# Optimization experiments

Hardware: AMD Instinct MI355X
Metric: run time of the kernel (lower is better)

Reference implementation:

```python
import jax, jax.numpy as jnp
import numpy as np
from jax import lax

N_NODES = 100000
N_EDGES = 1600000
FEAT = 8          # per-node feature dim
STATE = 4         # embed_dim
OUT = 16          # n classes
HID = 5           # hardcoded state_l1/output_l1
MAX_IT = 10


def setup_inputs() -> dict:
    key = jax.random.key(0)
    ks = jax.random.split(key, 12)
    edge_parent = jax.random.randint(ks[0], (N_EDGES,), 0, N_NODES, dtype=jnp.int32)
    edge_child = jax.random.randint(ks[1], (N_EDGES,), 0, N_NODES, dtype=jnp.int32)
    # arc_feat = inp[:, 1:] = [child_id, feat_parent, feat_child]  -> [E, 1+2F]
    feats = jax.random.normal(ks[2], (N_EDGES, 2 * FEAT), jnp.float32)
    arc_feat = jnp.concatenate([edge_child.astype(jnp.float32)[:, None], feats], axis=1)
    d_in = 1 + 2 * FEAT + STATE  # Net.state_input = input_dim - 1 + state_dim = 21
    std = 0.1  # truncated_normal(stddev=0.1) init in original
    W1 = std * jax.random.normal(ks[3], (d_in, HID), jnp.float32)
    b1 = jnp.zeros((HID,), jnp.float32)
    W2 = std * jax.random.normal(ks[4], (HID, STATE), jnp.float32)
    b2 = jnp.zeros((STATE,), jnp.float32)
    Wo1 = std * jax.random.normal(ks[5], (STATE, HID), jnp.float32)
    bo1 = jnp.zeros((HID,), jnp.float32)
    Wo2 = std * jax.random.normal(ks[6], (HID, OUT), jnp.float32)
    bo2 = jnp.zeros((OUT,), jnp.float32)
    return {
        'arc_feat': arc_feat, 'W1': W1, 'b1': b1, 'W2': W2, 'b2': b2,
        'Wo1': Wo1, 'bo1': bo1, 'Wo2': Wo2, 'bo2': bo2,
        'edge_parent': edge_parent, 'edge_child': edge_child,
        'n_nodes': N_NODES, 'max_it': MAX_IT,
    }


def reference(arc_feat, W1, b1, W2, b2, Wo1, bo1, Wo2, bo2,
              edge_parent, edge_child, n_nodes, max_it):
    state_dim = W2.shape[1]

    def step(state, _):
        gat = state[edge_child]                                  # [E, S] gather neighbor state
        x = jnp.concatenate([arc_feat, gat], axis=1)             # [E, D-1+S]
        h = jnp.tanh(x @ W1 + b1)                                # netSt layer1 [E, 5]
        m = jnp.tanh(h @ W2 + b2)                                # netSt layer2 [E, S]
        # sparse ArcNode @ m  == segment-sum edge messages to parent node
        new_state = jax.ops.segment_sum(m, edge_parent, num_segments=n_nodes)
        return new_state, None

    state0 = jnp.zeros((n_nodes, state_dim), arc_feat.dtype)
    state, _ = lax.scan(step, state0, None, length=max_it)       # fixed max_it iterations
    # netOut: node-based output (graph_based=False)
    ho = jnp.tanh(state @ Wo1 + bo1)                             # [N, 5]
    out = jax.nn.softmax(ho @ Wo2 + bo2, axis=-1)                # [N, OUT]
    return out
```

## Files before the change

### kernel.cpp

```cpp
#include <hip/hip_runtime.h>

#define N_NODES 100000
#define N_EDGES 1600000
#define STATE 4
#define OUT_C 16
#define HID 5
#define MAX_IT 10
#define ARC_D 17

__device__ __forceinline__ float fast_tanh(float x) {
    float e = __expf(2.0f * x);
    return 1.0f - 2.0f / (e + 1.0f);
}

__global__ void hist_kernel(const int* __restrict__ parent, int* __restrict__ counts, int E) {
    int e = blockIdx.x * blockDim.x + threadIdx.x;
    if (e < E) atomicAdd(&counts[parent[e]], 1);
}

#define SCAN_B 1024
__global__ __launch_bounds__(SCAN_B) void scanA(const int* __restrict__ counts,
                                                int* __restrict__ off,
                                                int* __restrict__ bsum, int n) {
    __shared__ int lds[SCAN_B];
    int t = threadIdx.x;
    int i = blockIdx.x * SCAN_B + t;
    int v = (i < n - 1) ? counts[i] : 0;
    lds[t] = v;
    for (int s = 1; s < SCAN_B; s <<= 1) {
        __syncthreads();
        int u = (t >= s) ? lds[t - s] : 0;
        __syncthreads();
        lds[t] += u;
    }
    __syncthreads();
    if (i < n) off[i] = lds[t] - v;
    if (t == SCAN_B - 1) bsum[blockIdx.x] = lds[t];
}

__global__ __launch_bounds__(128) void scanB(int* __restrict__ bsum, int nb) {
    __shared__ int lds[128];
    int t = threadIdx.x;
    int v = (t < nb) ? bsum[t] : 0;
    lds[t] = v;
    for (int s = 1; s < 128; s <<= 1) {
        __syncthreads();
        int u = (t >= s) ? lds[t - s] : 0;
        __syncthreads();
        lds[t] += u;
    }
    __syncthreads();
    if (t < nb) bsum[t] = lds[t] - v;
}

__global__ __launch_bounds__(SCAN_B) void scanC(int* __restrict__ off, const int* __restrict__ bsum,
                                                int* __restrict__ cursor, int n) {
    int i = blockIdx.x * SCAN_B + threadIdx.x;
    if (i < n) {
        int v = off[i] + bsum[blockIdx.x];
        off[i] = v;
        if (i < n - 1) cursor[i] = v;
    }
}

#define BBLK 256
__global__ __launch_bounds__(BBLK) void build_kernel(const float* __restrict__ arc,
                                                     const float* __restrict__ W1,
                                                     const float* __restrict__ b1,
                                                     const int* __restrict__ parent,
                                                     const int* __restrict__ child,
                                                     int* __restrict__ cursor,
                                                     float4* __restrict__ rec, int E) {
    __shared__ float lds[BBLK * ARC_D];
    int t = threadIdx.x;
    int base = blockIdx.x * BBLK;
    int cnt = E - base; if (cnt > BBLK) cnt = BBLK;
    for (int k = t; k < cnt * ARC_D; k += BBLK)
        lds[k] = arc[(size_t)base * ARC_D + k];
    __syncthreads();
    if (t < cnt) {
        int e = base + t;
        const float* row = &lds[t * ARC_D];
        float p[HID];
        #pragma unroll
        for (int j = 0; j < HID; ++j) p[j] = b1[j];
        #pragma unroll
        for (int i = 0; i < ARC_D; ++i) {
            float x = row[i];
            #pragma unroll
            for (int j = 0; j < HID; ++j) p[j] += x * W1[i * HID + j];
        }
        int pa = parent[e];
        int pos = atomicAdd(&cursor[pa], 1);
        rec[2 * (size_t)pos]     = make_float4(p[0], p[1], p[2], p[3]);
        rec[2 * (size_t)pos + 1] = make_float4(p[4], __uint_as_float((unsigned)child[e]),
                                               __uint_as_float((unsigned)pa), 0.0f);
    }
}

__global__ __launch_bounds__(256) void iter_kernel(const int* __restrict__ off,
                                                   const float4* __restrict__ rec,
                                                   const float* __restrict__ W1,
                                                   const float* __restrict__ W2,
                                                   const float* __restrict__ b2,
                                                   const float* __restrict__ src,
                                                   float* __restrict__ dst) {
    int tid = blockIdx.x * blockDim.x + threadIdx.x;
    int n  = tid >> 2;
    int sl = tid & 3;
    if (n >= N_NODES) return;
    float w1b[STATE][HID];
    #pragma unroll
    for (int k = 0; k < STATE; ++k)
        #pragma unroll
        for (int j = 0; j < HID; ++j) w1b[k][j] = W1[(ARC_D + k) * HID + j];
    float w2[HID][STATE];
    #pragma unroll
    for (int j = 0; j < HID; ++j)
        #pragma unroll
        for (int k = 0; k < STATE; ++k) w2[j][k] = W2[j * STATE + k];
    float b2v[STATE];
    #pragma unroll
    for (int k = 0; k < STATE; ++k) b2v[k] = b2[k];

    int s0 = off[n];
    int s1 = off[n + 1];
    float acc0 = 0.f, acc1 = 0.f, acc2 = 0.f, acc3 = 0.f;
    for (int i = s0 + sl; i < s1; i += 4) {
        float4 r0 = rec[2 * (size_t)i];
        float4 r1 = rec[2 * (size_t)i + 1];
        int c = (int)__float_as_uint(r1.y);
        float4 s = ((const float4*)src)[c];
        float p[HID] = {r0.x, r0.y, r0.z, r0.w};
        p[4] = r1.x;
        float h[HID];
        #pragma unroll
        for (int j = 0; j < HID; ++j) {
            float v = p[j] + s.x * w1b[0][j] + s.y * w1b[1][j]
                           + s.z * w1b[2][j] + s.w * w1b[3][j];
            h[j] = fast_tanh(v);
        }
        float m[STATE];
        #pragma unroll
        for (int k = 0; k < STATE; ++k) {
            float v = b2v[k];
            #pragma unroll
            for (int j = 0; j < HID; ++j) v += h[j] * w2[j][k];
            m[k] = fast_tanh(v);
        }
        acc0 += m[0]; acc1 += m[1]; acc2 += m[2]; acc3 += m[3];
    }
    acc0 += __shfl_xor(acc0, 1); acc0 += __shfl_xor(acc0, 2);
    acc1 += __shfl_xor(acc1, 1); acc1 += __shfl_xor(acc1, 2);
    acc2 += __shfl_xor(acc2, 1); acc2 += __shfl_xor(acc2, 2);
    acc3 += __shfl_xor(acc3, 1); acc3 += __shfl_xor(acc3, 2);
    if (sl == 0)
        ((float4*)dst)[n] = make_float4(acc0, acc1, acc2, acc3);
}

__global__ __launch_bounds__(256) void out_kernel(const float* __restrict__ state,
                                                  const float* __restrict__ Wo1,
                                                  const float* __restrict__ bo1,
                                                  const float* __restrict__ Wo2,
                                                  const float* __restrict__ bo2,
                                                  float* __restrict__ out) {
    int n = blockIdx.x * blockDim.x + threadIdx.x;
    if (n >= N_NODES) return;
    float4 s = ((const float4*)state)[n];
    float ho[HID];
    #pragma unroll
    for (int j = 0; j < HID; ++j) {
        float v = bo1[j] + s.x * Wo1[0 * HID + j] + s.y * Wo1[1 * HID + j]
                         + s.z * Wo1[2 * HID + j] + s.w * Wo1[3 * HID + j];
        ho[j] = fast_tanh(v);
    }
    float lg[OUT_C];
    float mx = -1e30f;
    #pragma unroll
    for (int o = 0; o < OUT_C; ++o) {
        float v = bo2[o];
        #pragma unroll
        for (int j = 0; j < HID; ++j) v += ho[j] * Wo2[j * OUT_C + o];
        lg[o] = v; mx = fmaxf(mx, v);
    }
    float sum = 0.f;
    #pragma unroll
    for (int o = 0; o < OUT_C; ++o) { lg[o] = __expf(lg[o] - mx); sum += lg[o]; }
    float inv = 1.0f / sum;
    float4* op = (float4*)&out[(size_t)n * OUT_C];
    op[0] = make_float4(lg[0] * inv, lg[1] * inv, lg[2] * inv, lg[3] * inv);
    op[1] = make_float4(lg[4] * inv, lg[5] * inv, lg[6] * inv, lg[7] * inv);
    op[2] = make_float4(lg[8] * inv, lg[9] * inv, lg[10] * inv, lg[11] * inv);
    op[3] = make_float4(lg[12] * inv, lg[13] * inv, lg[14] * inv, lg[15] * inv);
}

extern "C" void kernel_launch(void* const* d_in, const int* in_sizes, int n_in,
                              void* d_out, int out_size, void* d_ws, size_t ws_size,
                              hipStream_t stream) {
    const float* arc   = (const float*)d_in[0];
    const float* W1    = (const float*)d_in[1];
    const float* b1    = (const float*)d_in[2];
    const float* W2    = (const float*)d_in[3];
    const float* b2    = (const float*)d_in[4];
    const float* Wo1   = (const float*)d_in[5];
    const float* bo1   = (const float*)d_in[6];
    const float* Wo2   = (const float*)d_in[7];
    const float* bo2   = (const float*)d_in[8];
    const int* parent  = (const int*)d_in[9];
    const int* child   = (const int*)d_in[10];
    float* out = (float*)d_out;

    char* ws = (char*)d_ws;
    size_t o = 0;
    auto alloc = [&](size_t bytes) { void* p = ws + o; o += (bytes + 255) & ~255ULL; return p; };
    float4* rec   = (float4*)alloc((size_t)N_EDGES * 32);
    int*   counts = (int*)alloc((size_t)N_NODES * 4);
    int*   off    = (int*)alloc((size_t)(N_NODES + 1) * 4);
    int*   cursor = (int*)alloc((size_t)N_NODES * 4);
    int*   bsum   = (int*)alloc(1024 * 4);
    float* stateA = (float*)alloc((size_t)N_NODES * STATE * 4);
    float* stateB = (float*)alloc((size_t)N_NODES * STATE * 4);

    hipMemsetAsync(counts, 0, (size_t)N_NODES * 4, stream);
    hipMemsetAsync(stateA, 0, (size_t)N_NODES * STATE * 4, stream);

    hist_kernel<<<(N_EDGES + 255) / 256, 256, 0, stream>>>(parent, counts, N_EDGES);
    int n = N_NODES + 1;
    int nb = (n + SCAN_B - 1) / SCAN_B;
    scanA<<<nb, SCAN_B, 0, stream>>>(counts, off, bsum, n);
    scanB<<<1, 128, 0, stream>>>(bsum, nb);
    scanC<<<nb, SCAN_B, 0, stream>>>(off, bsum, cursor, n);
    build_kernel<<<(N_EDGES + BBLK - 1) / BBLK, BBLK, 0, stream>>>(arc, W1, b1, parent, child,
                                                                   cursor, rec, N_EDGES);
    float* src = stateA; float* dst = stateB;
    for (int it = 0; it < MAX_IT; ++it) {
        iter_kernel<<<(N_NODES * 4 + 255) / 256, 256, 0, stream>>>(off, rec, W1, W2, b2, src, dst);
        float* tmp = src; src = dst; dst = tmp;
    }
    out_kernel<<<(N_NODES + 255) / 256, 256, 0, stream>>>(src, Wo1, bo1, Wo2, bo2, out);
}
```

Baseline: 606.0 us.

## Switch iteration kernel to edge-parallel segmented scan with atomic flush

Replaces the node-parallel iteration kernel, which gave 4 threads per node, with one thread per edge over the parent-sorted records. Edges sharing a parent are combined by a wave-level segmented inclusive scan, and each segment tail atomically adds its sum into the destination state. Each iteration gets its own zeroed state buffer, so no per-iteration memset is needed. The aim is to remove load imbalance and idle lanes from varying node degrees. The cost is 4 atomics per segment, an 11x larger state workspace memset, and a 6-step shuffle scan on every edge.

```diff
diff --git a/kernel.cpp b/kernel.cpp
--- a/kernel.cpp
+++ b/kernel.cpp
@@ -98,17 +98,14 @@
     }
 }
 
-__global__ __launch_bounds__(256) void iter_kernel(const int* __restrict__ off,
-                                                   const float4* __restrict__ rec,
+__global__ __launch_bounds__(256) void iter_kernel(const float4* __restrict__ rec,
                                                    const float* __restrict__ W1,
                                                    const float* __restrict__ W2,
                                                    const float* __restrict__ b2,
                                                    const float* __restrict__ src,
-                                                   float* __restrict__ dst) {
-    int tid = blockIdx.x * blockDim.x + threadIdx.x;
-    int n  = tid >> 2;
-    int sl = tid & 3;
-    if (n >= N_NODES) return;
+                                                   float* __restrict__ dst, int E) {
+    int e = blockIdx.x * blockDim.x + threadIdx.x;
+    int lane = threadIdx.x & 63;
     float w1b[STATE][HID];
     #pragma unroll
     for (int k = 0; k < STATE; ++k)
@@ -123,39 +120,52 @@
     #pragma unroll
     for (int k = 0; k < STATE; ++k) b2v[k] = b2[k];
 
-    int s0 = off[n];
-    int s1 = off[n + 1];
-    float acc0 = 0.f, acc1 = 0.f, acc2 = 0.f, acc3 = 0.f;
-    for (int i = s0 + sl; i < s1; i += 4) {
-        float4 r0 = rec[2 * (size_t)i];
-        float4 r1 = rec[2 * (size_t)i + 1];
+    float m0 = 0.f, m1 = 0.f, m2 = 0.f, m3 = 0.f;
+    int p = -1;
+    if (e < E) {
+        float4 r0 = rec[2 * (size_t)e];
+        float4 r1 = rec[2 * (size_t)e + 1];
         int c = (int)__float_as_uint(r1.y);
+        p = (int)__float_as_uint(r1.z);
         float4 s = ((const float4*)src)[c];
-        float p[HID] = {r0.x, r0.y, r0.z, r0.w};
-        p[4] = r1.x;
+        float pr[HID] = {r0.x, r0.y, r0.z, r0.w};
+        pr[4] = r1.x;
         float h[HID];
         #pragma unroll
         for (int j = 0; j < HID; ++j) {
-            float v = p[j] + s.x * w1b[0][j] + s.y * w1b[1][j]
-                           + s.z * w1b[2][j] + s.w * w1b[3][j];
+            float v = pr[j] + s.x * w1b[0][j] + s.y * w1b[1][j]
+                            + s.z * w1b[2][j] + s.w * w1b[3][j];
             h[j] = fast_tanh(v);
         }
-        float m[STATE];
+        float mm[STATE];
         #pragma unroll
         for (int k = 0; k < STATE; ++k) {
             float v = b2v[k];
             #pragma unroll
             for (int j = 0; j < HID; ++j) v += h[j] * w2[j][k];
-            m[k] = fast_tanh(v);
+            mm[k] = fast_tanh(v);
         }
-        acc0 += m[0]; acc1 += m[1]; acc2 += m[2]; acc3 += m[3];
-    }
-    acc0 += __shfl_xor(acc0, 1); acc0 += __shfl_xor(acc0, 2);
-    acc1 += __shfl_xor(acc1, 1); acc1 += __shfl_xor(acc1, 2);
-    acc2 += __shfl_xor(acc2, 1); acc2 += __shfl_xor(acc2, 2);
-    acc3 += __shfl_xor(acc3, 1); acc3 += __shfl_xor(acc3, 2);
-    if (sl == 0)
-        ((float4*)dst)[n] = make_float4(acc0, acc1, acc2, acc3);
+        m0 = mm[0]; m1 = mm[1]; m2 = mm[2]; m3 = mm[3];
+    }
+    #pragma unroll
+    for (int d = 1; d < 64; d <<= 1) {
+        int   pp = __shfl_up(p, d);
+        float t0 = __shfl_up(m0, d);
+        float t1 = __shfl_up(m1, d);
+        float t2 = __shfl_up(m2, d);
+        float t3 = __shfl_up(m3, d);
+        bool ok = (lane >= d) && (pp == p);
+        if (ok) { m0 += t0; m1 += t1; m2 += t2; m3 += t3; }
+    }
+    int pn = __shfl_down(p, 1);
+    bool tail = (lane == 63) || (pn != p);
+    if (tail && e < E) {
+        float* d4 = &dst[(size_t)p * STATE];
+        atomicAdd(&d4[0], m0);
+        atomicAdd(&d4[1], m1);
+        atomicAdd(&d4[2], m2);
+        atomicAdd(&d4[3], m3);
+    }
 }
 
 __global__ __launch_bounds__(256) void out_kernel(const float* __restrict__ state,
@@ -214,15 +224,14 @@
     size_t o = 0;
     auto alloc = [&](size_t bytes) { void* p = ws + o; o += (bytes + 255) & ~255ULL; return p; };
     float4* rec   = (float4*)alloc((size_t)N_EDGES * 32);
+    float* states = (float*)alloc((size_t)(MAX_IT + 1) * N_NODES * STATE * 4);
     int*   counts = (int*)alloc((size_t)N_NODES * 4);
     int*   off    = (int*)alloc((size_t)(N_NODES + 1) * 4);
     int*   cursor = (int*)alloc((size_t)N_NODES * 4);
     int*   bsum   = (int*)alloc(1024 * 4);
-    float* stateA = (float*)alloc((size_t)N_NODES * STATE * 4);
-    float* stateB = (float*)alloc((size_t)N_NODES * STATE * 4);
 
     hipMemsetAsync(counts, 0, (size_t)N_NODES * 4, stream);
-    hipMemsetAsync(stateA, 0, (size_t)N_NODES * STATE * 4, stream);
+    hipMemsetAsync(states, 0, (size_t)(MAX_IT + 1) * N_NODES * STATE * 4, stream);
 
     hist_kernel<<<(N_EDGES + 255) / 256, 256, 0, stream>>>(parent, counts, N_EDGES);
     int n = N_NODES + 1;
@@ -232,10 +241,11 @@
     scanC<<<nb, SCAN_B, 0, stream>>>(off, bsum, cursor, n);
     build_kernel<<<(N_EDGES + BBLK - 1) / BBLK, BBLK, 0, stream>>>(arc, W1, b1, parent, child,
                                                                    cursor, rec, N_EDGES);
-    float* src = stateA; float* dst = stateB;
     for (int it = 0; it < MAX_IT; ++it) {
-        iter_kernel<<<(N_NODES * 4 + 255) / 256, 256, 0, stream>>>(off, rec, W1, W2, b2, src, dst);
-        float* tmp = src; src = dst; dst = tmp;
-    }
-    out_kernel<<<(N_NODES + 255) / 256, 256, 0, stream>>>(src, Wo1, bo1, Wo2, bo2, out);
-}
+        const float* src = states + (size_t)it * N_NODES * STATE;
+        float* dst = states + (size_t)(it + 1) * N_NODES * STATE;
+        iter_kernel<<<(N_EDGES + 255) / 256, 256, 0, stream>>>(rec, W1, W2, b2, src, dst, N_EDGES);
+    }
+    out_kernel<<<(N_NODES + 255) / 256, 256, 0, stream>>>(
+        states + (size_t)MAX_IT * N_NODES * STATE, Wo1, bo1, Wo2, bo2, out);
+}
```

After: 525.8 us. 13.2% less time.
